# Kernel optimization log

Measured on AMD Instinct MI355X. Metric: run time of the kernel, lower is better.

Reference implementation:

```python
import jax, jax.numpy as jnp
import numpy as np


def setup_inputs() -> dict:
    key = jax.random.key(0)
    ks = jax.random.split(key, 5)
    B, T, I, H, O = 64, 1024, 128, 256, 128
    stdv = 1.0 / np.sqrt(H)
    return {
        "x": jax.random.normal(ks[0], (B, T, I), dtype=jnp.float32),
        "W": jax.random.uniform(ks[1], (I, 4 * H), dtype=jnp.float32, minval=-stdv, maxval=stdv),
        "U": jax.random.uniform(ks[2], (H, 4 * H), dtype=jnp.float32, minval=-stdv, maxval=stdv),
        "bias": jax.random.uniform(ks[3], (4 * H,), dtype=jnp.float32, minval=-stdv, maxval=stdv),
        "dense_w": jax.random.uniform(ks[4], (O, H), dtype=jnp.float32, minval=-stdv, maxval=stdv),
        "dense_b": jnp.zeros((O,), dtype=jnp.float32),
    }


def reference(x, W, U, bias, dense_w, dense_b):
    B, T, I = x.shape
    H = U.shape[0]
    # Precompute input contribution for all timesteps in one big GEMM.
    xW = jnp.einsum("bti,ig->btg", x, W) + bias  # (B, T, 4H)

    def step(carry, xw_t):
        h, c = carry
        gates = xw_t + h @ U  # (B, 4H)
        i_t = jax.nn.sigmoid(gates[:, :H])
        f_t = jax.nn.sigmoid(gates[:, H:2 * H])
        g_t = jnp.tanh(gates[:, 2 * H:3 * H])
        o_t = jax.nn.sigmoid(gates[:, 3 * H:])
        c = f_t * c + i_t * g_t
        h = o_t * jnp.tanh(c)
        return (h, c), h

    h0 = jnp.zeros((B, H), dtype=x.dtype)
    c0 = jnp.zeros((B, H), dtype=x.dtype)
    (h_T, _), _ = jax.lax.scan(step, (h0, c0), jnp.swapaxes(xW, 0, 1))
    # Original takes hidden_seq[:, -1, :] == final h_t, then Linear, then unsqueeze(2).
    out = h_T @ dense_w.T + dense_b  # (B, O)
    return out[:, :, None]  # (B, O, 1)
```

## Files before the change

### kernel.cpp

```cpp
#include <hip/hip_runtime.h>
#include <math.h>

#define TT 1024
#define BB 64
#define II 128
#define HH 256
#define OO 128
#define KR 384
#define GPB 16
#define NCOL 64
#define Z_STRIDE 392
#define PART_BG_STRIDE 68
#define PART_RC_STRIDE 273

#define WS_HBUF_F 4096

__device__ __forceinline__ float rcp(float v) { return __builtin_amdgcn_rcpf(v); }
__device__ __forceinline__ float sigm(float v) { return rcp(1.f + __expf(-v)); }
__device__ __forceinline__ float ftanh(float v) {
    return __builtin_fmaf(-2.f, rcp(__expf(2.f * v) + 1.f), 1.f);
}

extern "C" __global__ void __launch_bounds__(256, 1) lstm_scan(
    const float* __restrict__ x, const float* __restrict__ W,
    const float* __restrict__ U, const float* __restrict__ bias,
    float* __restrict__ wsf)
{
    __shared__ float z[4 * Z_STRIDE];
    __shared__ float part[16 * PART_RC_STRIDE];
    __shared__ float gb[256];
    __shared__ float cst[64];
    __shared__ float bia[64];
    __shared__ int   misc[8];

    int*   flags  = (int*)wsf;
    int*   abortp = ((int*)wsf) + 2048;
    float* hbuf   = wsf + WS_HBUF_F;

    const int tid = threadIdx.x;
    const int gid = blockIdx.x & 15;
    const int p   = blockIdx.x >> 4;
    const int cg  = tid & 15;
    const int rc  = tid >> 4;

    float wr[6][4][4];
    {
        const int c0 = cg * 4;
        const int gate = c0 >> 4, j = c0 & 15;
        const int gcol = gate * HH + p * 16 + j;
#pragma unroll
        for (int rr = 0; rr < 6; ++rr) {
#pragma unroll
            for (int i = 0; i < 4; ++i) {
                const int r = rr * 64 + rc * 4 + i;
                const float4 wv = (rr < 2)
                    ? *(const float4*)(W + (size_t)r * 1024 + gcol)
                    : *(const float4*)(U + (size_t)(r - II) * 1024 + gcol);
                wr[rr][i][0] = wv.x; wr[rr][i][1] = wv.y;
                wr[rr][i][2] = wv.z; wr[rr][i][3] = wv.w;
            }
        }
    }

    if (tid < NCOL) {
        int gate = tid >> 4, j = tid & 15;
        bia[tid] = bias[gate * HH + p * 16 + j];
    }
    if (tid < 64) cst[tid] = 0.f;
    for (int idx = tid; idx < 4 * Z_STRIDE; idx += 256) z[idx] = 0.f;
    if (tid < 8) misc[tid] = 0;

    const int lane = tid & 63;
    const int bgw  = tid >> 6;

    if (tid < 128) {
        const int b2 = tid >> 5, l2 = tid & 31;
        const float4 xv = *(const float4*)(
            x + ((size_t)(4 * gid + b2) * TT + 0) * II + 4 * l2);
        *(float4*)(z + b2 * Z_STRIDE + 4 * l2) = xv;
    }
    __syncthreads();

    for (int t = 1; t <= TT; ++t) {
        float acc[4][4];
#pragma unroll
        for (int a = 0; a < 4; ++a)
#pragma unroll
            for (int b = 0; b < 4; ++b) acc[a][b] = 0.f;

#pragma unroll
        for (int rr = 0; rr < 2; ++rr) {
#pragma unroll
            for (int bg = 0; bg < 4; ++bg) {
                const float4 zv = *(const float4*)(z + bg * Z_STRIDE + rr * 64 + rc * 4);
#pragma unroll
                for (int c = 0; c < 4; ++c)
                    acc[bg][c] += zv.x * wr[rr][0][c] + zv.y * wr[rr][1][c]
                                + zv.z * wr[rr][2][c] + zv.w * wr[rr][3][c];
            }
        }

        if (t > 1) {
            if (tid < 64) {
                const int need = t - 1;
                const int* fp = &flags[((lane & 15) * 16 + gid) * 8];
                int it = 0, ab = 0;
                for (;;) {
                    int f1 = need, f2 = need;
                    if (lane < GPB) {
                        f1 = __hip_atomic_load(fp, __ATOMIC_RELAXED,
                                               __HIP_MEMORY_SCOPE_AGENT);
                        f2 = __hip_atomic_load(fp, __ATOMIC_RELAXED,
                                               __HIP_MEMORY_SCOPE_AGENT);
                    }
                    if (__ballot(f1 >= need) == ~0ULL) break;
                    if (__ballot(f2 >= need) == ~0ULL) break;
                    if ((++it & 63) == 0) {
                        int abv = __hip_atomic_load(abortp, __ATOMIC_RELAXED,
                                                    __HIP_MEMORY_SCOPE_AGENT);
                        if (abv) { ab = 1; break; }
                        if (it > (1 << 19)) {
                            if (lane == 0)
                                __hip_atomic_store(abortp, 1, __ATOMIC_RELAXED,
                                                   __HIP_MEMORY_SCOPE_AGENT);
                            ab = 1; break;
                        }
                    }
                }
                if (lane == 0) misc[1] = ab;
            }
            __syncthreads();
            asm volatile("" ::: "memory");
            if (misc[1]) break;

            const float* hsrc = hbuf + ((size_t)((t - 1) & 1) * BB + 4 * gid + bgw) * HH;
            const float v0 = __hip_atomic_load(hsrc + lane,       __ATOMIC_RELAXED, __HIP_MEMORY_SCOPE_AGENT);
            const float v1 = __hip_atomic_load(hsrc + lane + 64,  __ATOMIC_RELAXED, __HIP_MEMORY_SCOPE_AGENT);
            const float v2 = __hip_atomic_load(hsrc + lane + 128, __ATOMIC_RELAXED, __HIP_MEMORY_SCOPE_AGENT);
            const float v3 = __hip_atomic_load(hsrc + lane + 192, __ATOMIC_RELAXED, __HIP_MEMORY_SCOPE_AGENT);
            float* zdst = z + bgw * Z_STRIDE + II + lane;
            zdst[0]   = v0;
            zdst[64]  = v1;
            zdst[128] = v2;
            zdst[192] = v3;
        }
        __syncthreads();

#pragma unroll
        for (int rr = 2; rr < 6; ++rr) {
#pragma unroll
            for (int bg = 0; bg < 4; ++bg) {
                const float4 zv = *(const float4*)(z + bg * Z_STRIDE + rr * 64 + rc * 4);
#pragma unroll
                for (int c = 0; c < 4; ++c)
                    acc[bg][c] += zv.x * wr[rr][0][c] + zv.y * wr[rr][1][c]
                                + zv.z * wr[rr][2][c] + zv.w * wr[rr][3][c];
            }
        }

#pragma unroll
        for (int bg = 0; bg < 4; ++bg)
#pragma unroll
            for (int c = 0; c < 4; ++c)
                part[rc * PART_RC_STRIDE + bg * PART_BG_STRIDE + cg * 4 + c] = acc[bg][c];
        __syncthreads();

        {
            const int bg = tid >> 6, col = tid & 63;
            float s = 0.f;
#pragma unroll
            for (int r2 = 0; r2 < 16; ++r2)
                s += part[r2 * PART_RC_STRIDE + bg * PART_BG_STRIDE + col];
            gb[bg * 64 + col] = s + bia[col];
        }
        __syncthreads();

        if (tid < 64) {
            const int bg = tid >> 4, j = tid & 15;
            const float gi = gb[bg * 64 + j];
            const float gf = gb[bg * 64 + 16 + j];
            const float gg = gb[bg * 64 + 32 + j];
            const float go = gb[bg * 64 + 48 + j];
            const float iv = sigm(gi);
            const float fv = sigm(gf);
            const float gv = ftanh(gg);
            const float ov = sigm(go);
            const float cv = fv * cst[tid] + iv * gv;
            cst[tid] = cv;
            const float hv = ov * ftanh(cv);
            __hip_atomic_store(
                hbuf + ((size_t)(t & 1) * BB + 4 * gid + bg) * HH + p * 16 + j,
                hv, __ATOMIC_RELAXED, __HIP_MEMORY_SCOPE_AGENT);
        } else if (tid >= 128 && t < TT) {
            const int i2 = tid - 128;
            const int b2 = i2 >> 5, l2 = i2 & 31;
            const float4 xv = *(const float4*)(
                x + ((size_t)(4 * gid + b2) * TT + t) * II + 4 * l2);
            *(float4*)(z + b2 * Z_STRIDE + 4 * l2) = xv;
        }
        asm volatile("" ::: "memory");
        __syncthreads();
        if (tid == 0)
            __hip_atomic_store(&flags[blockIdx.x * 8], t,
                               __ATOMIC_RELAXED, __HIP_MEMORY_SCOPE_AGENT);
    }
}

extern "C" __global__ void __launch_bounds__(256) lstm_out(
    const float* __restrict__ wsf, const float* __restrict__ dw,
    const float* __restrict__ db, float* __restrict__ out)
{
    __shared__ float hs[256];
    __shared__ float red[256];
    const int b = blockIdx.x;
    const int tid = threadIdx.x;
    const float* h0 = wsf + WS_HBUF_F;
    hs[tid] = h0[(size_t)b * HH + tid];
    __syncthreads();
    const int o = tid & 127, half = tid >> 7;
    const float* wrow = dw + o * HH + half * 128;
    const float* hrow = hs + half * 128;
    float s = 0.f;
#pragma unroll
    for (int k = 0; k < 128; k += 4) {
        const float4 wv = *(const float4*)(wrow + k);
        s += hrow[k] * wv.x + hrow[k + 1] * wv.y + hrow[k + 2] * wv.z + hrow[k + 3] * wv.w;
    }
    red[tid] = s;
    __syncthreads();
    if (tid < 128)
        out[(size_t)b * OO + tid] = red[tid] + red[128 + tid] + db[tid];
}

extern "C" void kernel_launch(void* const* d_in, const int* in_sizes, int n_in,
                              void* d_out, int out_size, void* d_ws, size_t ws_size,
                              hipStream_t stream)
{
    const float* x    = (const float*)d_in[0];
    const float* W    = (const float*)d_in[1];
    const float* U    = (const float*)d_in[2];
    const float* bias = (const float*)d_in[3];
    const float* dw   = (const float*)d_in[4];
    const float* db   = (const float*)d_in[5];
    float* out = (float*)d_out;
    float* ws  = (float*)d_ws;

    hipMemsetAsync(d_ws, 0, 16384, stream);
    hipLaunchKernelGGL(lstm_scan, dim3(256), dim3(256), 0, stream,
                       x, W, U, bias, ws);
    hipLaunchKernelGGL(lstm_out, dim3(64), dim3(256), 0, stream, ws, dw, db, out);
}
```

Before: 2.419 ms.

## Use per-wave flags and fuse gate reduction with cell update via shuffles

Result: slower. 2.483 ms (+2.7%).

```diff
diff --git a/kernel.cpp b/kernel.cpp
--- a/kernel.cpp
+++ b/kernel.cpp
@@ -6,14 +6,14 @@
 #define II 128
 #define HH 256
 #define OO 128
-#define KR 384
 #define GPB 16
 #define NCOL 64
 #define Z_STRIDE 392
 #define PART_BG_STRIDE 68
 #define PART_RC_STRIDE 273
 
-#define WS_HBUF_F 4096
+#define WS_HBUF_F 8192
+#define WS_CLEAR_B 20480
 
 __device__ __forceinline__ float rcp(float v) { return __builtin_amdgcn_rcpf(v); }
 __device__ __forceinline__ float sigm(float v) { return rcp(1.f + __expf(-v)); }
@@ -28,26 +28,25 @@
 {
     __shared__ float z[4 * Z_STRIDE];
     __shared__ float part[16 * PART_RC_STRIDE];
-    __shared__ float gb[256];
-    __shared__ float cst[64];
-    __shared__ float bia[64];
     __shared__ int   misc[8];
 
     int*   flags  = (int*)wsf;
-    int*   abortp = ((int*)wsf) + 2048;
+    int*   abortp = ((int*)wsf) + 4096;
     float* hbuf   = wsf + WS_HBUF_F;
 
-    const int tid = threadIdx.x;
-    const int gid = blockIdx.x & 15;
-    const int p   = blockIdx.x >> 4;
-    const int cg  = tid & 15;
-    const int rc  = tid >> 4;
+    const int tid  = threadIdx.x;
+    const int gid  = blockIdx.x & 15;
+    const int p    = blockIdx.x >> 4;
+    const int cg   = tid & 15;
+    const int rc   = tid >> 4;
+    const int lane = tid & 63;
+    const int w    = tid >> 6;
+    const int myb  = 4 * gid + w;
 
     float wr[6][4][4];
     {
         const int c0 = cg * 4;
-        const int gate = c0 >> 4, j = c0 & 15;
-        const int gcol = gate * HH + p * 16 + j;
+        const int gcol = (c0 >> 4) * HH + p * 16 + (c0 & 15);
 #pragma unroll
         for (int rr = 0; rr < 6; ++rr) {
 #pragma unroll
@@ -61,17 +60,11 @@
             }
         }
     }
-
-    if (tid < NCOL) {
-        int gate = tid >> 4, j = tid & 15;
-        bia[tid] = bias[gate * HH + p * 16 + j];
-    }
-    if (tid < 64) cst[tid] = 0.f;
+    const float bia_reg = bias[(lane >> 4) * HH + p * 16 + (lane & 15)];
+    float creg = 0.f;
+
     for (int idx = tid; idx < 4 * Z_STRIDE; idx += 256) z[idx] = 0.f;
     if (tid < 8) misc[tid] = 0;
-
-    const int lane = tid & 63;
-    const int bgw  = tid >> 6;
 
     if (tid < 128) {
         const int b2 = tid >> 5, l2 = tid & 31;
@@ -101,50 +94,44 @@
         }
 
         if (t > 1) {
-            if (tid < 64) {
-                const int need = t - 1;
-                const int* fp = &flags[((lane & 15) * 16 + gid) * 8];
-                int it = 0, ab = 0;
-                for (;;) {
-                    int f1 = need, f2 = need;
-                    if (lane < GPB) {
-                        f1 = __hip_atomic_load(fp, __ATOMIC_RELAXED,
+            const int need = t - 1;
+            const int* fp = &flags[((lane & 15) * GPB + gid) * 16 + w * 4];
+            int it = 0;
+            for (;;) {
+                int f1 = need, f2 = need;
+                if (lane < GPB) {
+                    f1 = __hip_atomic_load(fp, __ATOMIC_RELAXED, __HIP_MEMORY_SCOPE_AGENT);
+                    f2 = __hip_atomic_load(fp, __ATOMIC_RELAXED, __HIP_MEMORY_SCOPE_AGENT);
+                }
+                if (__ballot(f1 >= need) == ~0ULL) break;
+                if (__ballot(f2 >= need) == ~0ULL) break;
+                if ((++it & 63) == 0) {
+                    int abv = __hip_atomic_load(abortp, __ATOMIC_RELAXED,
+                                                __HIP_MEMORY_SCOPE_AGENT);
+                    if (abv) { if (lane == 0) misc[w] = 1; break; }
+                    if (it > (1 << 19)) {
+                        if (lane == 0) {
+                            __hip_atomic_store(abortp, 1, __ATOMIC_RELAXED,
                                                __HIP_MEMORY_SCOPE_AGENT);
-                        f2 = __hip_atomic_load(fp, __ATOMIC_RELAXED,
-                                               __HIP_MEMORY_SCOPE_AGENT);
-                    }
-                    if (__ballot(f1 >= need) == ~0ULL) break;
-                    if (__ballot(f2 >= need) == ~0ULL) break;
-                    if ((++it & 63) == 0) {
-                        int abv = __hip_atomic_load(abortp, __ATOMIC_RELAXED,
-                                                    __HIP_MEMORY_SCOPE_AGENT);
-                        if (abv) { ab = 1; break; }
-                        if (it > (1 << 19)) {
-                            if (lane == 0)
-                                __hip_atomic_store(abortp, 1, __ATOMIC_RELAXED,
-                                                   __HIP_MEMORY_SCOPE_AGENT);
-                            ab = 1; break;
+                            misc[w] = 1;
                         }
+                        break;
                     }
                 }
-                if (lane == 0) misc[1] = ab;
-            }
-            __syncthreads();
-            asm volatile("" ::: "memory");
-            if (misc[1]) break;
-
-            const float* hsrc = hbuf + ((size_t)((t - 1) & 1) * BB + 4 * gid + bgw) * HH;
+            }
+            const float* hsrc = hbuf + ((size_t)((t - 1) & 1) * BB + myb) * HH;
             const float v0 = __hip_atomic_load(hsrc + lane,       __ATOMIC_RELAXED, __HIP_MEMORY_SCOPE_AGENT);
             const float v1 = __hip_atomic_load(hsrc + lane + 64,  __ATOMIC_RELAXED, __HIP_MEMORY_SCOPE_AGENT);
             const float v2 = __hip_atomic_load(hsrc + lane + 128, __ATOMIC_RELAXED, __HIP_MEMORY_SCOPE_AGENT);
             const float v3 = __hip_atomic_load(hsrc + lane + 192, __ATOMIC_RELAXED, __HIP_MEMORY_SCOPE_AGENT);
-            float* zdst = z + bgw * Z_STRIDE + II + lane;
+            float* zdst = z + w * Z_STRIDE + II + lane;
             zdst[0]   = v0;
             zdst[64]  = v1;
             zdst[128] = v2;
             zdst[192] = v3;
         }
         __syncthreads();
+        if (misc[0] | misc[1] | misc[2] | misc[3]) break;
 
 #pragma unroll
         for (int rr = 2; rr < 6; ++rr) {
@@ -165,44 +152,38 @@
                 part[rc * PART_RC_STRIDE + bg * PART_BG_STRIDE + cg * 4 + c] = acc[bg][c];
         __syncthreads();
 
-        {
-            const int bg = tid >> 6, col = tid & 63;
-            float s = 0.f;
-#pragma unroll
-            for (int r2 = 0; r2 < 16; ++r2)
-                s += part[r2 * PART_RC_STRIDE + bg * PART_BG_STRIDE + col];
-            gb[bg * 64 + col] = s + bia[col];
+        float s = bia_reg;
+#pragma unroll
+        for (int r2 = 0; r2 < 16; ++r2)
+            s += part[r2 * PART_RC_STRIDE + w * PART_BG_STRIDE + lane];
+
+        const int j = lane & 15;
+        const float sf = __shfl(s, j + 16);
+        const float sg = __shfl(s, j + 32);
+        const float so = __shfl(s, j + 48);
+        if (lane < 16) {
+            const float iv = sigm(s);
+            const float fv = sigm(sf);
+            const float gv = ftanh(sg);
+            const float ov = sigm(so);
+            creg = fv * creg + iv * gv;
+            const float hv = ov * ftanh(creg);
+            __hip_atomic_store(
+                hbuf + ((size_t)(t & 1) * BB + myb) * HH + p * 16 + j,
+                hv, __ATOMIC_RELAXED, __HIP_MEMORY_SCOPE_AGENT);
+        }
+        asm volatile("s_waitcnt vmcnt(0)" ::: "memory");
+        if (lane == 0)
+            __hip_atomic_store(&flags[blockIdx.x * 16 + w * 4], t,
+                               __ATOMIC_RELAXED, __HIP_MEMORY_SCOPE_AGENT);
+
+        if (t < TT && lane >= 16 && lane < 48) {
+            const int l2 = lane - 16;
+            const float4 xv = *(const float4*)(
+                x + ((size_t)myb * TT + t) * II + 4 * l2);
+            *(float4*)(z + w * Z_STRIDE + 4 * l2) = xv;
         }
         __syncthreads();
-
-        if (tid < 64) {
-            const int bg = tid >> 4, j = tid & 15;
-            const float gi = gb[bg * 64 + j];
-            const float gf = gb[bg * 64 + 16 + j];
-            const float gg = gb[bg * 64 + 32 + j];
-            const float go = gb[bg * 64 + 48 + j];
-            const float iv = sigm(gi);
-            const float fv = sigm(gf);
-            const float gv = ftanh(gg);
-            const float ov = sigm(go);
-            const float cv = fv * cst[tid] + iv * gv;
-            cst[tid] = cv;
-            const float hv = ov * ftanh(cv);
-            __hip_atomic_store(
-                hbuf + ((size_t)(t & 1) * BB + 4 * gid + bg) * HH + p * 16 + j,
-                hv, __ATOMIC_RELAXED, __HIP_MEMORY_SCOPE_AGENT);
-        } else if (tid >= 128 && t < TT) {
-            const int i2 = tid - 128;
-            const int b2 = i2 >> 5, l2 = i2 & 31;
-            const float4 xv = *(const float4*)(
-                x + ((size_t)(4 * gid + b2) * TT + t) * II + 4 * l2);
-            *(float4*)(z + b2 * Z_STRIDE + 4 * l2) = xv;
-        }
-        asm volatile("" ::: "memory");
-        __syncthreads();
-        if (tid == 0)
-            __hip_atomic_store(&flags[blockIdx.x * 8], t,
-                               __ATOMIC_RELAXED, __HIP_MEMORY_SCOPE_AGENT);
     }
 }
 
@@ -245,7 +226,7 @@
     float* out = (float*)d_out;
     float* ws  = (float*)d_ws;
 
-    hipMemsetAsync(d_ws, 0, 16384, stream);
+    hipMemsetAsync(d_ws, 0, WS_CLEAR_B, stream);
     hipLaunchKernelGGL(lstm_scan, dim3(256), dim3(256), 0, stream,
                        x, W, U, bias, ws);
     hipLaunchKernelGGL(lstm_out, dim3(64), dim3(256), 0, stream, ws, dw, db, out);
```
